# Optimization experiments

Hardware: AMD Instinct MI355X
Metric: run time of the kernel (lower is better)

The kernel has to match this reference:

```python
import jax, jax.numpy as jnp
import numpy as np

EMB_DIM = 256
NUM_RELATIONS = 128
BATCH = 4096
LOG_SQRT_2PI = 0.9189385332046727  # 0.5*log(2*pi)


def setup_inputs() -> dict:
    key = jax.random.key(0)
    k1, k2, k3, k4, k5 = jax.random.split(key, 5)
    sbjs = jax.random.normal(k1, (BATCH, EMB_DIM), dtype=jnp.float32)
    objs = jax.random.normal(k2, (BATCH, EMB_DIM), dtype=jnp.float32)
    mus = jax.random.normal(k3, (NUM_RELATIONS, 2 * EMB_DIM), dtype=jnp.float32)
    sigmas = jnp.abs(jax.random.normal(k4, (NUM_RELATIONS, 2 * EMB_DIM), dtype=jnp.float32)) + 1.0
    relation_priors = jax.random.normal(k5, (NUM_RELATIONS,), dtype=jnp.float32)
    return {"sbjs": sbjs, "objs": objs, "mus": mus, "sigmas": sigmas,
            "relation_priors": relation_priors}


def reference(sbjs, objs, mus, sigmas, relation_priors):
    # x: [B, 2D] concatenated subject/object embeddings
    x = jnp.concatenate([sbjs, objs], axis=1)
    two_d = x.shape[1]
    # Gaussian log-pdf, broadcast over relations: [B, R, 2D]
    z = (x[:, None, :] - mus[None, :, :]) / sigmas[None, :, :]
    logp = -0.5 * z * z - jnp.log(sigmas)[None, :, :] - LOG_SQRT_2PI
    # Original adds prior to every one of the 2D dims before the sum,
    # so the prior contributes prior * 2D to each [b, r] output.
    return logp.sum(axis=-1) + relation_priors[None, :] * two_d
```

## Files before the change

kernel.cpp:

```cpp
#include <hip/hip_runtime.h>
#include <hip/hip_bf16.h>
#include <cstddef>
#include <cstdint>

#define EMB   256
#define TWOD  512
#define NREL  128
#define BATCH 4096
#define LOG_SQRT_2PI 0.9189385332046727f

typedef __bf16          bf16x8  __attribute__((ext_vector_type(8)));
typedef unsigned short  u16x8   __attribute__((ext_vector_type(8)));
typedef float           f32x4   __attribute__((ext_vector_type(4)));

__device__ __forceinline__ unsigned short f2bf(float f) {
    unsigned u = __builtin_bit_cast(unsigned, f);
    u = (u + 0x7FFFu + ((u >> 16) & 1u)) >> 16;
    return (unsigned short)u;
}

__device__ __forceinline__ bf16x8 pack8(float4 a, float4 b) {
    u16x8 u;
    u[0] = f2bf(a.x); u[1] = f2bf(a.y); u[2] = f2bf(a.z); u[3] = f2bf(a.w);
    u[4] = f2bf(b.x); u[5] = f2bf(b.y); u[6] = f2bf(b.z); u[7] = f2bf(b.w);
    return __builtin_bit_cast(bf16x8, u);
}

__device__ __forceinline__ void gl_lds16(const void* g, void* l) {
    __builtin_amdgcn_global_load_lds(
        (const __attribute__((address_space(1))) unsigned int*)g,
        (__attribute__((address_space(3))) unsigned int*)l, 16, 0, 0);
}

__global__ __launch_bounds__(256) void nb_prep(
    const float* __restrict__ mus, const float* __restrict__ sigmas,
    const float* __restrict__ priors,
    unsigned short* __restrict__ Wc, unsigned short* __restrict__ Wa,
    float* __restrict__ cst)
{
    const int r = blockIdx.x;
    const int tid = threadIdx.x;
    float esum = 0.0f;
    #pragma unroll
    for (int i = 0; i < 2; i++) {
        const int k = tid + i * 256;
        const float mu = mus[r * TWOD + k];
        const float s  = sigmas[r * TWOD + k];
        const float inv2 = 1.0f / (s * s);
        esum += -0.5f * mu * mu * inv2 - logf(s) - LOG_SQRT_2PI;
        const int idx = (k >> 3) * (NREL * 8) + r * 8 + (k & 7);
        Wc[idx] = f2bf(mu * inv2);
        Wa[idx] = f2bf(-0.5f * inv2);
    }
    __shared__ float red[4];
    #pragma unroll
    for (int off = 32; off >= 1; off >>= 1)
        esum += __shfl_down(esum, off, 64);
    if ((tid & 63) == 0) red[tid >> 6] = esum;
    __syncthreads();
    if (tid == 0)
        cst[r] = red[0] + red[1] + red[2] + red[3] + priors[r] * (float)TWOD;
}

#define CHP  8
#define NCHK 8

__device__ __forceinline__ void issue_chunk(
    unsigned short* sW, const unsigned short* Wc, const unsigned short* Wa,
    int wv, int lane, int ch, int buf)
{
    const int t = wv & 1;
    const unsigned short* g = t ? Wa : Wc;
    const int pbase = (wv >> 1) * 4;
    #pragma unroll
    for (int j = 0; j < 4; j++) {
        #pragma unroll
        for (int h = 0; h < 2; h++) {
            const int p    = pbase + j;
            const int goff = (ch * CHP + p) * 1024 + h * 512 + lane * 8;
            const int loff = buf * 16384 + t * 8192 + p * 1024 + h * 512;
            gl_lds16(g + goff, &sW[loff]);
        }
    }
}

__global__ __launch_bounds__(256, 1) void nb_fused(
    const float* __restrict__ sbjs, const float* __restrict__ objs,
    const unsigned short* __restrict__ Wc, const unsigned short* __restrict__ Wa,
    const float* __restrict__ cst, float* __restrict__ out)
{
    __shared__ unsigned short sW[2 * 2 * CHP * 1024];

    const int tid  = threadIdx.x;
    const int wv   = tid >> 6;
    const int lane = tid & 63;
    const int m16  = lane & 15;
    const int quad = lane >> 4;
    const int b0   = blockIdx.x * 16;

    issue_chunk(sW, Wc, Wa, wv, lane, 0, 0);

    bf16x8 ax[16], ax2[16];
    {
        const int row = b0 + m16;
        #pragma unroll
        for (int fi = 0; fi < 16; fi++) {
            const int col = fi * 32 + quad * 8;
            const float* p = (col < EMB)
                ? (sbjs + (size_t)row * EMB + col)
                : (objs + (size_t)row * EMB + (col - EMB));
            const float4 v0 = *(const float4*)p;
            const float4 v1 = *(const float4*)(p + 4);
            ax[fi] = pack8(v0, v1);
            const float4 s0 = {v0.x * v0.x, v0.y * v0.y, v0.z * v0.z, v0.w * v0.w};
            const float4 s1 = {v1.x * v1.x, v1.y * v1.y, v1.z * v1.z, v1.w * v1.w};
            ax2[fi] = pack8(s0, s1);
        }
    }

    f32x4 acc[2];
    acc[0] = (f32x4)0.0f;
    acc[1] = (f32x4)0.0f;

    __syncthreads();

    #pragma unroll
    for (int ch = 0; ch < NCHK; ch++) {
        const int buf = ch & 1;
        if (ch + 1 < NCHK)
            issue_chunk(sW, Wc, Wa, wv, lane, ch + 1, buf ^ 1);

        #pragma unroll
        for (int ks2 = 0; ks2 < 2; ks2++) {
            const int fi = ch * 2 + ks2;
            const int pb = buf * 16384 + (ks2 * 4 + quad) * 1024;
            #pragma unroll
            for (int nt = 0; nt < 2; nt++) {
                const int r  = wv * 32 + nt * 16 + m16;
                const bf16x8 bc = *(const bf16x8*)&sW[pb + r * 8];
                const bf16x8 ba = *(const bf16x8*)&sW[pb + 8192 + r * 8];
                acc[nt] = __builtin_amdgcn_mfma_f32_16x16x32_bf16(
                              ax[fi],  bc, acc[nt], 0, 0, 0);
                acc[nt] = __builtin_amdgcn_mfma_f32_16x16x32_bf16(
                              ax2[fi], ba, acc[nt], 0, 0, 0);
            }
        }
        __syncthreads();
    }

    #pragma unroll
    for (int nt = 0; nt < 2; nt++) {
        const int r = wv * 32 + nt * 16 + m16;
        const float ca = cst[r];
        #pragma unroll
        for (int reg = 0; reg < 4; reg++)
            out[(size_t)(b0 + quad * 4 + reg) * NREL + r] = acc[nt][reg] + ca;
    }
}

__global__ __launch_bounds__(256) void nb_slow(
    const float* __restrict__ sbjs, const float* __restrict__ objs,
    const float* __restrict__ mus, const float* __restrict__ sigmas,
    const float* __restrict__ priors, float* __restrict__ out)
{
    const int idx = blockIdx.x * 256 + threadIdx.x;
    const int b = idx >> 7;
    const int r = idx & (NREL - 1);
    float acc = priors[r] * (float)TWOD;
    for (int k = 0; k < TWOD; k++) {
        const float x  = (k < EMB) ? sbjs[(size_t)b * EMB + k]
                                   : objs[(size_t)b * EMB + (k - EMB)];
        const float mu = mus[r * TWOD + k];
        const float s  = sigmas[r * TWOD + k];
        const float z  = (x - mu) / s;
        acc += -0.5f * z * z - logf(s) - LOG_SQRT_2PI;
    }
    out[idx] = acc;
}

extern "C" void kernel_launch(void* const* d_in, const int* in_sizes, int n_in,
                              void* d_out, int out_size, void* d_ws, size_t ws_size,
                              hipStream_t stream)
{
    const float* sbjs   = (const float*)d_in[0];
    const float* objs   = (const float*)d_in[1];
    const float* mus    = (const float*)d_in[2];
    const float* sigmas = (const float*)d_in[3];
    const float* priors = (const float*)d_in[4];
    float* out = (float*)d_out;

    char* ws = (char*)d_ws;
    const size_t o_wc  = 0;
    const size_t o_wa  = 256 << 10;
    const size_t o_cst = 512 << 10;
    const size_t need  = o_cst + NREL * sizeof(float);

    if (ws_size >= need) {
        unsigned short* Wcp = (unsigned short*)(ws + o_wc);
        unsigned short* Wap = (unsigned short*)(ws + o_wa);
        float* cst = (float*)(ws + o_cst);
        nb_prep<<<NREL, 256, 0, stream>>>(mus, sigmas, priors, Wcp, Wap, cst);
        nb_fused<<<BATCH / 16, 256, 0, stream>>>(sbjs, objs, Wcp, Wap, cst, out);
    } else {
        nb_slow<<<(BATCH * NREL) / 256, 256, 0, stream>>>(
            sbjs, objs, mus, sigmas, priors, out);
    }
}
```

Before: 73.47 us.

## Interleave weight tables and read them directly from global instead of LDS staging

The prep kernel now writes the Wc and Wa weights interleaved into one buffer, using 64 threads per relation with vectorized loads and a single-wave reduction. The fused kernel drops the double-buffered global-to-LDS pipeline and its barriers, loading the B operands straight from global memory (served by L2) into registers. It also splits the accumulator into two independent MFMA chains to shorten dependency stalls. The risk is higher global/L2 traffic and latency exposure, because every block re-reads the full weight table without explicit prefetch.

Result: no change. 72.44 us (-1.4%).

```diff
diff --git a/kernel.cpp b/kernel.cpp
--- a/kernel.cpp
+++ b/kernel.cpp
@@ -26,126 +26,85 @@
     return __builtin_bit_cast(bf16x8, u);
 }
 
-__device__ __forceinline__ void gl_lds16(const void* g, void* l) {
-    __builtin_amdgcn_global_load_lds(
-        (const __attribute__((address_space(1))) unsigned int*)g,
-        (__attribute__((address_space(3))) unsigned int*)l, 16, 0, 0);
-}
-
-__global__ __launch_bounds__(256) void nb_prep(
+__global__ __launch_bounds__(64) void nb_prep(
     const float* __restrict__ mus, const float* __restrict__ sigmas,
     const float* __restrict__ priors,
-    unsigned short* __restrict__ Wc, unsigned short* __restrict__ Wa,
-    float* __restrict__ cst)
+    unsigned short* __restrict__ Wi, float* __restrict__ cst)
 {
-    const int r = blockIdx.x;
-    const int tid = threadIdx.x;
+    const int r  = blockIdx.x;
+    const int k8 = threadIdx.x;
+    const float* mp = mus    + (size_t)r * TWOD + k8 * 8;
+    const float* sp = sigmas + (size_t)r * TWOD + k8 * 8;
+    const float4 m0 = *(const float4*)mp,       m1 = *(const float4*)(mp + 4);
+    const float4 s0 = *(const float4*)sp,       s1 = *(const float4*)(sp + 4);
+
+    float mu[8] = {m0.x, m0.y, m0.z, m0.w, m1.x, m1.y, m1.z, m1.w};
+    float sg[8] = {s0.x, s0.y, s0.z, s0.w, s1.x, s1.y, s1.z, s1.w};
+
+    u16x8 pc, pa;
     float esum = 0.0f;
     #pragma unroll
-    for (int i = 0; i < 2; i++) {
-        const int k = tid + i * 256;
-        const float mu = mus[r * TWOD + k];
-        const float s  = sigmas[r * TWOD + k];
-        const float inv2 = 1.0f / (s * s);
-        esum += -0.5f * mu * mu * inv2 - logf(s) - LOG_SQRT_2PI;
-        const int idx = (k >> 3) * (NREL * 8) + r * 8 + (k & 7);
-        Wc[idx] = f2bf(mu * inv2);
-        Wa[idx] = f2bf(-0.5f * inv2);
+    for (int i = 0; i < 8; i++) {
+        const float inv2 = 1.0f / (sg[i] * sg[i]);
+        pc[i] = f2bf(mu[i] * inv2);
+        pa[i] = f2bf(-0.5f * inv2);
+        esum += -0.5f * mu[i] * mu[i] * inv2 - __logf(sg[i]) - LOG_SQRT_2PI;
     }
-    __shared__ float red[4];
+    unsigned short* w = Wi + (size_t)k8 * (NREL * 16) + r * 16;
+    *(u16x8*)w       = pc;
+    *(u16x8*)(w + 8) = pa;
+
     #pragma unroll
     for (int off = 32; off >= 1; off >>= 1)
         esum += __shfl_down(esum, off, 64);
-    if ((tid & 63) == 0) red[tid >> 6] = esum;
-    __syncthreads();
-    if (tid == 0)
-        cst[r] = red[0] + red[1] + red[2] + red[3] + priors[r] * (float)TWOD;
-}
-
-#define CHP  8
-#define NCHK 8
-
-__device__ __forceinline__ void issue_chunk(
-    unsigned short* sW, const unsigned short* Wc, const unsigned short* Wa,
-    int wv, int lane, int ch, int buf)
-{
-    const int t = wv & 1;
-    const unsigned short* g = t ? Wa : Wc;
-    const int pbase = (wv >> 1) * 4;
-    #pragma unroll
-    for (int j = 0; j < 4; j++) {
-        #pragma unroll
-        for (int h = 0; h < 2; h++) {
-            const int p    = pbase + j;
-            const int goff = (ch * CHP + p) * 1024 + h * 512 + lane * 8;
-            const int loff = buf * 16384 + t * 8192 + p * 1024 + h * 512;
-            gl_lds16(g + goff, &sW[loff]);
-        }
-    }
+    if (k8 == 0) cst[r] = esum + priors[r] * (float)TWOD;
 }
 
 __global__ __launch_bounds__(256, 1) void nb_fused(
     const float* __restrict__ sbjs, const float* __restrict__ objs,
-    const unsigned short* __restrict__ Wc, const unsigned short* __restrict__ Wa,
+    const unsigned short* __restrict__ Wi,
     const float* __restrict__ cst, float* __restrict__ out)
 {
-    __shared__ unsigned short sW[2 * 2 * CHP * 1024];
-
     const int tid  = threadIdx.x;
     const int wv   = tid >> 6;
     const int lane = tid & 63;
     const int m16  = lane & 15;
     const int quad = lane >> 4;
     const int b0   = blockIdx.x * 16;
-
-    issue_chunk(sW, Wc, Wa, wv, lane, 0, 0);
+    const int row  = b0 + m16;
 
     bf16x8 ax[16], ax2[16];
-    {
-        const int row = b0 + m16;
-        #pragma unroll
-        for (int fi = 0; fi < 16; fi++) {
-            const int col = fi * 32 + quad * 8;
-            const float* p = (col < EMB)
-                ? (sbjs + (size_t)row * EMB + col)
-                : (objs + (size_t)row * EMB + (col - EMB));
-            const float4 v0 = *(const float4*)p;
-            const float4 v1 = *(const float4*)(p + 4);
-            ax[fi] = pack8(v0, v1);
-            const float4 s0 = {v0.x * v0.x, v0.y * v0.y, v0.z * v0.z, v0.w * v0.w};
-            const float4 s1 = {v1.x * v1.x, v1.y * v1.y, v1.z * v1.z, v1.w * v1.w};
-            ax2[fi] = pack8(s0, s1);
-        }
+    #pragma unroll
+    for (int fi = 0; fi < 16; fi++) {
+        const int col = fi * 32 + quad * 8;
+        const float* p = (col < EMB)
+            ? (sbjs + (size_t)row * EMB + col)
+            : (objs + (size_t)row * EMB + (col - EMB));
+        const float4 v0 = *(const float4*)p;
+        const float4 v1 = *(const float4*)(p + 4);
+        ax[fi] = pack8(v0, v1);
+        const float4 q0 = {v0.x * v0.x, v0.y * v0.y, v0.z * v0.z, v0.w * v0.w};
+        const float4 q1 = {v1.x * v1.x, v1.y * v1.y, v1.z * v1.z, v1.w * v1.w};
+        ax2[fi] = pack8(q0, q1);
     }
 
-    f32x4 acc[2];
-    acc[0] = (f32x4)0.0f;
-    acc[1] = (f32x4)0.0f;
+    f32x4 accc[2], acca[2];
+    accc[0] = (f32x4)0.0f; accc[1] = (f32x4)0.0f;
+    acca[0] = (f32x4)0.0f; acca[1] = (f32x4)0.0f;
 
-    __syncthreads();
-
+    const unsigned short* wbase = Wi + (size_t)quad * (NREL * 16)
+                                     + (wv * 32 + m16) * 16;
     #pragma unroll
-    for (int ch = 0; ch < NCHK; ch++) {
-        const int buf = ch & 1;
-        if (ch + 1 < NCHK)
-            issue_chunk(sW, Wc, Wa, wv, lane, ch + 1, buf ^ 1);
-
-        #pragma unroll
-        for (int ks2 = 0; ks2 < 2; ks2++) {
-            const int fi = ch * 2 + ks2;
-            const int pb = buf * 16384 + (ks2 * 4 + quad) * 1024;
-            #pragma unroll
-            for (int nt = 0; nt < 2; nt++) {
-                const int r  = wv * 32 + nt * 16 + m16;
-                const bf16x8 bc = *(const bf16x8*)&sW[pb + r * 8];
-                const bf16x8 ba = *(const bf16x8*)&sW[pb + 8192 + r * 8];
-                acc[nt] = __builtin_amdgcn_mfma_f32_16x16x32_bf16(
-                              ax[fi],  bc, acc[nt], 0, 0, 0);
-                acc[nt] = __builtin_amdgcn_mfma_f32_16x16x32_bf16(
-                              ax2[fi], ba, acc[nt], 0, 0, 0);
-            }
-        }
-        __syncthreads();
+    for (int fi = 0; fi < 16; fi++) {
+        const unsigned short* wp = wbase + (size_t)fi * 4 * (NREL * 16);
+        const bf16x8 bc0 = *(const bf16x8*)(wp);
+        const bf16x8 ba0 = *(const bf16x8*)(wp + 8);
+        const bf16x8 bc1 = *(const bf16x8*)(wp + 256);
+        const bf16x8 ba1 = *(const bf16x8*)(wp + 264);
+        accc[0] = __builtin_amdgcn_mfma_f32_16x16x32_bf16(ax [fi], bc0, accc[0], 0, 0, 0);
+        acca[0] = __builtin_amdgcn_mfma_f32_16x16x32_bf16(ax2[fi], ba0, acca[0], 0, 0, 0);
+        accc[1] = __builtin_amdgcn_mfma_f32_16x16x32_bf16(ax [fi], bc1, accc[1], 0, 0, 0);
+        acca[1] = __builtin_amdgcn_mfma_f32_16x16x32_bf16(ax2[fi], ba1, acca[1], 0, 0, 0);
     }
 
     #pragma unroll
@@ -154,7 +113,8 @@
         const float ca = cst[r];
         #pragma unroll
         for (int reg = 0; reg < 4; reg++)
-            out[(size_t)(b0 + quad * 4 + reg) * NREL + r] = acc[nt][reg] + ca;
+            out[(size_t)(b0 + quad * 4 + reg) * NREL + r] =
+                accc[nt][reg] + acca[nt][reg] + ca;
     }
 }
 
@@ -190,17 +150,15 @@
     float* out = (float*)d_out;
 
     char* ws = (char*)d_ws;
-    const size_t o_wc  = 0;
-    const size_t o_wa  = 256 << 10;
-    const size_t o_cst = 512 << 10;
+    const size_t o_w   = 0;
+    const size_t o_cst = 256 << 10;
     const size_t need  = o_cst + NREL * sizeof(float);
 
     if (ws_size >= need) {
-        unsigned short* Wcp = (unsigned short*)(ws + o_wc);
-        unsigned short* Wap = (unsigned short*)(ws + o_wa);
+        unsigned short* Wi = (unsigned short*)(ws + o_w);
         float* cst = (float*)(ws + o_cst);
-        nb_prep<<<NREL, 256, 0, stream>>>(mus, sigmas, priors, Wcp, Wap, cst);
-        nb_fused<<<BATCH / 16, 256, 0, stream>>>(sbjs, objs, Wcp, Wap, cst, out);
+        nb_prep<<<NREL, 64, 0, stream>>>(mus, sigmas, priors, Wi, cst);
+        nb_fused<<<BATCH / 16, 256, 0, stream>>>(sbjs, objs, Wi, cst, out);
     } else {
         nb_slow<<<(BATCH * NREL) / 256, 256, 0, stream>>>(
             sbjs, objs, mus, sigmas, priors, out);
```
